# Optimization experiments

Hardware: AMD Instinct MI355X
Metric: run time of the kernel (lower is better)

## Reference

```python
import jax, jax.numpy as jnp
import numpy as np

B, N, EMB, HID, CODE, FEAT, L = 8, 96, 768, 384, 192, 768, 2
NEG = 1e30  # mask_logic constant


def _gru(x, h, Wih, Whh, bih, bhh):
    # torch.nn.GRUCell math; gate order r, z, n
    gi = x @ Wih.T + bih
    gh = h @ Whh.T + bhh
    ir, iz, inn = jnp.split(gi, 3, axis=-1)
    hr, hz, hn = jnp.split(gh, 3, axis=-1)
    r = jax.nn.sigmoid(ir + hr)
    z = jax.nn.sigmoid(iz + hz)
    n = jnp.tanh(inn + r * hn)
    return (1.0 - z) * n + z * h


def _node0(Hl, gc, gp):
    # node 0: C = gru_c(x, 0); P = gru_p(0, x); H1 = C + P
    x0 = Hl[:, 0]
    z0 = jnp.zeros_like(x0)
    h0 = _gru(x0, z0, *gc) + _gru(z0, x0, *gp)
    b, n, d = Hl.shape
    return jnp.zeros((b, n, d), Hl.dtype).at[:, 0].set(h0)


def _dag_scan(Hl, s_mask, aux, Wr0, Wr1, gc, gp, get_w):
    # sequential DAG recurrence: node i attends over nodes < i of the CURRENT layer's outputs
    b, n, d = Hl.shape
    buf0 = _node0(Hl, gc, gp)
    pos = jnp.arange(n)

    def step(buf, inp):
        i, q, s_row, aux_row = inp
        valid = pos < i                                  # growing history slice [:i]
        w = get_w(buf, q, aux_row, valid)                # (B,N), zero for j >= i
        s = s_row[:, :, None]
        V = (buf @ Wr0.T) * s + (buf @ Wr1.T) * (1.0 - s)  # speaker-relation values
        M = jnp.einsum('bn,bnd->bd', w, V)
        hn = _gru(q, M, *gc) + _gru(M, q, *gp)           # C + P
        return buf.at[:, i].set(hn), w

    xs = (jnp.arange(1, n),
          jnp.swapaxes(Hl[:, 1:], 0, 1),
          jnp.swapaxes(s_mask[:, 1:], 0, 1),
          jnp.swapaxes(aux[:, 1:], 0, 1))
    buf, ws = jax.lax.scan(step, buf0, xs)
    return buf, jnp.swapaxes(ws, 0, 1)  # H1 (B,N,D), attn rows 1..N-1 (B,N-1,N)


def _mlp(x, W0, b0, W1, b1):
    # out_mlp with mlp_layers=1 (dropout is identity in eval mode)
    return jax.nn.relu(x @ W0.T + b0) @ W1.T + b1


def _forward(features, adj, s_mask, s_mask_onehot,
             enc_fc1_W, enc_fc1_b, enc_gat_w, enc_gat_b, enc_Wr0, enc_Wr1,
             enc_gruc_Wih, enc_gruc_Whh, enc_gruc_bih, enc_gruc_bhh,
             enc_grup_Wih, enc_grup_Whh, enc_grup_bih, enc_grup_bhh,
             enc_mlp_W0, enc_mlp_b0, enc_mlp_W1, enc_mlp_b1,
             dec_fc1_W, dec_fc1_b, dec_Wr0, dec_Wr1,
             dec_gruc_Wih, dec_gruc_Whh, dec_gruc_bih, dec_gruc_bhh,
             dec_grup_Wih, dec_grup_Whh, dec_grup_bih, dec_grup_bhh,
             dec_mlp_W0, dec_mlp_b0, dec_mlp_W1, dec_mlp_b1,
             lengths):
    b, n, _ = features.shape
    I = jnp.broadcast_to(jnp.eye(n, dtype=features.dtype), (b, n, n))
    # ----- encoder -----
    Hs = [jax.nn.relu(features @ enc_fc1_W.T + enc_fc1_b)]
    adjB_list = [jnp.zeros((b, 1, n), features.dtype)]
    for l in range(L):
        gc = (enc_gruc_Wih[l], enc_gruc_Whh[l], enc_gruc_bih[l], enc_gruc_bhh[l])
        gp = (enc_grup_Wih[l], enc_grup_Whh[l], enc_grup_bih[l], enc_grup_bhh[l])
        wq, wk, gb = enc_gat_w[l, :HID], enc_gat_w[l, HID:], enc_gat_b[l]

        def get_w(buf, q, adj_row, valid, wq=wq, wk=wk, gb=gb):
            # GAT_encoder: alpha = Linear([q; K]) masked by adj over history (mask_logic)
            alpha = buf @ wk + (q @ wq)[:, None] + gb
            alpha = alpha - (1.0 - adj_row) * NEG
            alpha = jnp.where(valid[None, :], alpha, -jnp.inf)
            return jax.nn.softmax(alpha, axis=-1)

        H1, ws = _dag_scan(Hs[l], s_mask, adj, enc_Wr0[l], enc_Wr1[l], gc, gp, get_w)
        Hs.append(H1)
        # row 0 of adjB is zeros; rows 1..N-1 are zero-padded attention weights
        adjB_list.append(jnp.concatenate([jnp.zeros((b, 1, n), features.dtype), ws], axis=1))
    fU = _mlp(jnp.concatenate(Hs, axis=-1), enc_mlp_W0, enc_mlp_b0, enc_mlp_W1, enc_mlp_b1)
    # ----- decoder -----
    Hs = [jax.nn.relu(fU @ dec_fc1_W.T + dec_fc1_b)]
    for l in range(L):
        gc = (dec_gruc_Wih[l], dec_gruc_Whh[l], dec_gruc_bih[l], dec_gruc_bhh[l])
        gp = (dec_grup_Wih[l], dec_grup_Whh[l], dec_grup_bih[l], dec_grup_bhh[l])
        b_inv = jnp.linalg.solve(I, I - adjB_list[l + 1])

        def get_w(buf, q, w_row, valid):
            # GNN_decoder: uses b_inv[:, i, :i] directly as gather weights
            return jnp.where(valid[None, :], w_row, 0.0)

        H1, _ = _dag_scan(Hs[l], s_mask, b_inv, dec_Wr0[l], dec_Wr1[l], gc, gp, get_w)
        Hs.append(H1)
    logits = _mlp(jnp.concatenate(Hs, axis=-1), dec_mlp_W0, dec_mlp_b0, dec_mlp_W1, dec_mlp_b1)
    feature_map = jnp.linalg.solve(I, I - adjB_list[2])
    return logits, feature_map


def setup_inputs() -> dict:
    key = jax.random.key(0)
    ks = iter(jax.random.split(key, 48))

    def rn(*shape):
        return jax.random.normal(next(ks), shape, jnp.float32) * 0.05

    return dict(
        features=jax.random.normal(next(ks), (B, N, EMB), jnp.float32),
        adj=jax.random.randint(next(ks), (B, N, N), 0, 2).astype(jnp.float32),
        s_mask=jax.random.randint(next(ks), (B, N, N), 0, 2).astype(jnp.float32),
        s_mask_onehot=jnp.zeros((B, N, N, 2), jnp.float32),
        lengths=jax.random.randint(next(ks), (B,), 1, N),
        enc_fc1_W=rn(HID, EMB), enc_fc1_b=rn(HID),
        enc_gat_w=rn(L, 2 * HID), enc_gat_b=rn(L),
        enc_Wr0=rn(L, HID, HID), enc_Wr1=rn(L, HID, HID),
        enc_gruc_Wih=rn(L, 3 * HID, HID), enc_gruc_Whh=rn(L, 3 * HID, HID),
        enc_gruc_bih=rn(L, 3 * HID), enc_gruc_bhh=rn(L, 3 * HID),
        enc_grup_Wih=rn(L, 3 * HID, HID), enc_grup_Whh=rn(L, 3 * HID, HID),
        enc_grup_bih=rn(L, 3 * HID), enc_grup_bhh=rn(L, 3 * HID),
        enc_mlp_W0=rn(HID, (L + 1) * HID), enc_mlp_b0=rn(HID),
        enc_mlp_W1=rn(CODE, HID), enc_mlp_b1=rn(CODE),
        dec_fc1_W=rn(HID, CODE), dec_fc1_b=rn(HID),
        dec_Wr0=rn(L, HID, HID), dec_Wr1=rn(L, HID, HID),
        dec_gruc_Wih=rn(L, 3 * HID, HID), dec_gruc_Whh=rn(L, 3 * HID, HID),
        dec_gruc_bih=rn(L, 3 * HID), dec_gruc_bhh=rn(L, 3 * HID),
        dec_grup_Wih=rn(L, 3 * HID, HID), dec_grup_Whh=rn(L, 3 * HID, HID),
        dec_grup_bih=rn(L, 3 * HID), dec_grup_bhh=rn(L, 3 * HID),
        dec_mlp_W0=rn(HID, (L + 1) * HID), dec_mlp_b0=rn(HID),
        dec_mlp_W1=rn(FEAT, HID), dec_mlp_b1=rn(FEAT),
    )


def reference(features, adj, s_mask, s_mask_onehot, lengths,
              enc_fc1_W, enc_fc1_b, enc_gat_w, enc_gat_b, enc_Wr0, enc_Wr1,
              enc_gruc_Wih, enc_gruc_Whh, enc_gruc_bih, enc_gruc_bhh,
              enc_grup_Wih, enc_grup_Whh, enc_grup_bih, enc_grup_bhh,
              enc_mlp_W0, enc_mlp_b0, enc_mlp_W1, enc_mlp_b1,
              dec_fc1_W, dec_fc1_b, dec_Wr0, dec_Wr1,
              dec_gruc_Wih, dec_gruc_Whh, dec_gruc_bih, dec_gruc_bhh,
              dec_grup_Wih, dec_grup_Whh, dec_grup_bih, dec_grup_bhh,
              dec_mlp_W0, dec_mlp_b0, dec_mlp_W1, dec_mlp_b1):
    return _forward(features, adj, s_mask, s_mask_onehot,
                    enc_fc1_W, enc_fc1_b, enc_gat_w, enc_gat_b, enc_Wr0, enc_Wr1,
                    enc_gruc_Wih, enc_gruc_Whh, enc_gruc_bih, enc_gruc_bhh,
                    enc_grup_Wih, enc_grup_Whh, enc_grup_bih, enc_grup_bhh,
                    enc_mlp_W0, enc_mlp_b0, enc_mlp_W1, enc_mlp_b1,
                    dec_fc1_W, dec_fc1_b, dec_Wr0, dec_Wr1,
                    dec_gruc_Wih, dec_gruc_Whh, dec_gruc_bih, dec_gruc_bhh,
                    dec_grup_Wih, dec_grup_Whh, dec_grup_bih, dec_grup_bhh,
                    dec_mlp_W0, dec_mlp_b0, dec_mlp_W1, dec_mlp_b1,
                    lengths)
```

## Files before the change

### kernel.cpp

```cpp
#include <hip/hip_runtime.h>
#include <math.h>

#define B_    8
#define N_    96
#define EMB_  768
#define HID_  384
#define GID_  1152
#define CONC_ 1152
#define CODE_ 192
#define FEAT_ 768
#define NSL_  64
#define SD_   6
#define NRW_  42

__device__ __forceinline__ float sigf(float x) { return 1.0f / (1.0f + expf(-x)); }

__device__ __forceinline__ void atstf(float* p, float v) {
  __hip_atomic_store(p, v, __ATOMIC_RELAXED, __HIP_MEMORY_SCOPE_AGENT);
}
__device__ __forceinline__ float atldf(const float* p) {
  return __hip_atomic_load((float*)p, __ATOMIC_RELAXED, __HIP_MEMORY_SCOPE_AGENT);
}
__device__ __forceinline__ float dot4(float4 a, float4 b) {
  return fmaf(a.x, b.x, fmaf(a.y, b.y, fmaf(a.z, b.z, a.w * b.w)));
}

template<int RELU>
__global__ __launch_bounds__(256)
void gemm_bias(const float* __restrict__ A, int lda,
               const float* __restrict__ W,
               const float* __restrict__ bias,
               float* __restrict__ C, int ldc, int K)
{
  __shared__ float As[16][68];
  __shared__ float Bs[16][68];
  const int tid = threadIdx.x;
  const int m0 = blockIdx.y * 64;
  const int n0 = blockIdx.x * 64;
  const int lr = tid >> 2;
  const int lc = (tid & 3) * 4;
  const int ty = tid >> 4, tx = tid & 15;
  float acc[4][4] = {};
  for (int k0 = 0; k0 < K; k0 += 16) {
    float4 a4 = *(const float4*)(A + (size_t)(m0 + lr) * lda + k0 + lc);
    float4 b4 = *(const float4*)(W + (size_t)(n0 + lr) * K + k0 + lc);
    As[lc+0][lr] = a4.x; As[lc+1][lr] = a4.y; As[lc+2][lr] = a4.z; As[lc+3][lr] = a4.w;
    Bs[lc+0][lr] = b4.x; Bs[lc+1][lr] = b4.y; Bs[lc+2][lr] = b4.z; Bs[lc+3][lr] = b4.w;
    __syncthreads();
#pragma unroll
    for (int k = 0; k < 16; ++k) {
      float av[4], bv[4];
#pragma unroll
      for (int i = 0; i < 4; ++i) av[i] = As[k][ty*4+i];
#pragma unroll
      for (int j = 0; j < 4; ++j) bv[j] = Bs[k][tx*4+j];
#pragma unroll
      for (int i = 0; i < 4; ++i)
#pragma unroll
        for (int j = 0; j < 4; ++j) acc[i][j] = fmaf(av[i], bv[j], acc[i][j]);
    }
    __syncthreads();
  }
#pragma unroll
  for (int i = 0; i < 4; ++i) {
    int m = m0 + ty*4 + i;
#pragma unroll
    for (int j = 0; j < 4; ++j) {
      int n = n0 + tx*4 + j;
      float v = acc[i][j] + bias[n];
      if (RELU) v = fmaxf(v, 0.0f);
      C[(size_t)m * ldc + n] = v;
    }
  }
}

__global__ __launch_bounds__(256)
void prod_kernel(const float* __restrict__ Ac, const float* __restrict__ Ap,
                 const float* __restrict__ W0, const float* __restrict__ W1,
                 float* __restrict__ G)
{
  const float* A = (blockIdx.z < 2) ? Ac : Ap;
  const float* W = (blockIdx.z & 1) ? W1 : W0;
  float* C = G + (size_t)blockIdx.z * GID_ * HID_;
  __shared__ float As[16][68];
  __shared__ float Bs[16][68];
  const int tid = threadIdx.x;
  const int m0 = blockIdx.y * 64;
  const int n0 = blockIdx.x * 64;
  const int lr = tid >> 2;
  const int lc = (tid & 3) * 4;
  const int lr2 = tid & 63, kq = tid >> 6;
  const int ty = tid >> 4, tx = tid & 15;
  float acc[4][4] = {};
  for (int k0 = 0; k0 < HID_; k0 += 16) {
    float4 a4 = *(const float4*)(A + (size_t)(m0 + lr) * HID_ + k0 + lc);
    As[lc+0][lr] = a4.x; As[lc+1][lr] = a4.y; As[lc+2][lr] = a4.z; As[lc+3][lr] = a4.w;
#pragma unroll
    for (int u = 0; u < 4; ++u) {
      int kl = kq * 4 + u;
      Bs[kl][lr2] = W[(size_t)(k0 + kl) * HID_ + n0 + lr2];
    }
    __syncthreads();
#pragma unroll
    for (int k = 0; k < 16; ++k) {
      float av[4], bv[4];
#pragma unroll
      for (int i = 0; i < 4; ++i) av[i] = As[k][ty*4+i];
#pragma unroll
      for (int j = 0; j < 4; ++j) bv[j] = Bs[k][tx*4+j];
#pragma unroll
      for (int i = 0; i < 4; ++i)
#pragma unroll
        for (int j = 0; j < 4; ++j) acc[i][j] = fmaf(av[i], bv[j], acc[i][j]);
    }
    __syncthreads();
  }
#pragma unroll
  for (int i = 0; i < 4; ++i)
#pragma unroll
    for (int j = 0; j < 4; ++j)
      C[(size_t)(m0 + ty*4 + i) * HID_ + n0 + tx*4 + j] = acc[i][j];
}

struct ScanP {
  const float* __restrict__ Hl;
  float*       __restrict__ bufC;
  float*       __restrict__ hnX;
  const float* __restrict__ G;
  const float* __restrict__ GIc;
  const float* __restrict__ GHp;
  const float* __restrict__ bhhc;
  const float* __restrict__ bihp;
  const float* __restrict__ Wr0;
  const float* __restrict__ Wr1;
  const float* __restrict__ wk;
  const float* __restrict__ mask;
  const float* __restrict__ smask;
  float*       __restrict__ adjB;
};

template<int ENC>
__global__ __launch_bounds__(256, 2)
void scan_kernel(ScanP p)
{
  const int tid  = threadIdx.x;
  const int bid  = blockIdx.x;
  const int b    = (bid >> 3) & 7;
  const int sl   = ((bid & 7) << 3) | (bid >> 6);
  const int j0   = sl * SD_;
  const int team = tid >> 4, lane = tid & 15;

  __shared__ __align__(16) float stage[HID_];
  __shared__ float ws0[N_], ws1[N_], s_sm[N_];
  __shared__ float alpha[N_];
  __shared__ float dots[48];
  __shared__ float red4[4];
  __shared__ float sh_aknew;
  __shared__ float PA[NRW_ * 97];
  __shared__ float PB[NRW_ * 97];

  for (int k = tid; k < NRW_ * 97; k += 256) { PA[k] = 0.f; PB[k] = 0.f; }

  float4 wAr[3][6], wBr[3][6];
#pragma unroll
  for (int u = 0; u < 3; ++u) {
    const int r = team + 16 * u;
    const float *Aptr, *Bptr;
    if (r < 36) {
      const int g = r / 6, jl = r % 6;
      const size_t off = (size_t)((g % 3) * HID_ + j0 + jl) * HID_;
      const float* base = p.G + (g < 3 ? 0 : 2) * (size_t)GID_ * HID_;
      Aptr = base + off;
      Bptr = base + (size_t)GID_ * HID_ + off;
    } else if (r < 42) {
      const int jl = r - 36;
      Aptr = p.Wr0 + (size_t)(j0 + jl) * HID_;
      Bptr = p.Wr1 + (size_t)(j0 + jl) * HID_;
    } else if (r == 42 && ENC) {
      Aptr = p.wk; Bptr = p.wk;
    } else {
      Aptr = p.Wr0; Bptr = p.Wr1;
    }
#pragma unroll
    for (int m = 0; m < 6; ++m) {
      wAr[u][m] = ((const float4*)Aptr)[lane + 16*m];
      wBr[u][m] = ((const float4*)Bptr)[lane + 16*m];
    }
  }
  float bh0=0, bh1=0, bh2=0, bi0=0, bi1=0, bi2=0;
  if (tid < SD_) {
    int j = j0 + tid;
    bh0 = p.bhhc[j]; bh1 = p.bhhc[HID_ + j]; bh2 = p.bhhc[2*HID_ + j];
    bi0 = p.bihp[j]; bi1 = p.bihp[HID_ + j]; bi2 = p.bihp[2*HID_ + j];
  }

#define BULK_STAGE(SRC)                                                      \
  do {                                                                       \
    if (tid < NSL_) {                                                        \
      const float* f_ = (SRC) + tid * SD_;                                   \
      while (__float_as_uint(atldf(f_)) == 0xFFFFFFFFu) {}                   \
    }                                                                        \
    __syncthreads();                                                         \
    {                                                                        \
      float v0 = atldf((SRC) + tid);                                         \
      while (__float_as_uint(v0) == 0xFFFFFFFFu) v0 = atldf((SRC) + tid);    \
      stage[tid] = v0;                                                       \
      if (tid < HID_ - 256) {                                                \
        float v1 = atldf((SRC) + 256 + tid);                                 \
        while (__float_as_uint(v1) == 0xFFFFFFFFu)                           \
          v1 = atldf((SRC) + 256 + tid);                                     \
        stage[256 + tid] = v1;                                               \
      }                                                                      \
    }                                                                        \
    __syncthreads();                                                         \
  } while (0)

  if (tid < SD_) {
    int j = j0 + tid;
    const float* gi = p.GIc + (size_t)(b * N_) * GID_;
    const float* gh = p.GHp + (size_t)(b * N_) * GID_;
    float rc = sigf(gi[j] + bh0);
    float zc = sigf(gi[HID_ + j] + bh1);
    float nc = tanhf(gi[2*HID_ + j] + rc * bh2);
    float outc = (1.0f - zc) * nc;
    float rp = sigf(bi0 + gh[j]);
    float zp = sigf(bi1 + gh[HID_ + j]);
    float np = tanhf(bi2 + rp * gh[2*HID_ + j]);
    float x0 = p.Hl[(size_t)(b * N_) * CONC_ + j];
    float h0 = outc + (1.0f - zp) * np + zp * x0;
    p.bufC[(size_t)(b * N_) * CONC_ + j] = h0;
    atstf(&p.hnX[(size_t)(b * N_) * HID_ + j], h0);
  }
  __syncthreads();

  for (int i = 1; i < N_; ++i) {
    float pf_gi0=0, pf_gi1=0, pf_gi2=0, pf_gh0=0, pf_gh1=0, pf_gh2=0, pf_q=0;
    if (tid < SD_) {
      int j = j0 + tid;
      const float* gi = p.GIc + ((size_t)b * N_ + i) * GID_;
      const float* gh = p.GHp + ((size_t)b * N_ + i) * GID_;
      pf_gi0 = gi[j]; pf_gi1 = gi[HID_ + j]; pf_gi2 = gi[2*HID_ + j];
      pf_gh0 = gh[j]; pf_gh1 = gh[HID_ + j]; pf_gh2 = gh[2*HID_ + j];
      pf_q   = p.Hl[((size_t)b * N_ + i) * CONC_ + j];
    }
    float pf_mrow = 0.0f;
    if (tid < N_) {
      pf_mrow = p.mask[((size_t)b * N_ + i) * N_ + tid];
      s_sm[tid] = p.smask[((size_t)b * N_ + i) * N_ + tid];
    }

    const float* srcH = p.hnX + (size_t)(b * N_ + (i - 1)) * HID_;
    BULK_STAGE(srcH);
    const float4* st4 = (const float4*)stage;
    float4 hreg[6];
#pragma unroll
    for (int m = 0; m < 6; ++m) hreg[m] = st4[lane + 16*m];

#pragma unroll
    for (int u = 0; u < 3; ++u) {
      const int r = team + 16 * u;
      float a = 0.f, bv = 0.f;
#pragma unroll
      for (int m = 0; m < 6; ++m) {
        a  += dot4(wAr[u][m], hreg[m]);
        bv += dot4(wBr[u][m], hreg[m]);
      }
#pragma unroll
      for (int mm = 8; mm; mm >>= 1) {
        a  += __shfl_xor(a, mm);
        bv += __shfl_xor(bv, mm);
      }
      if (lane == 0) {
        if (r < NRW_) { PA[r * 97 + (i - 1)] = a; PB[r * 97 + (i - 1)] = bv; }
        else if (ENC && r == 42) sh_aknew = a;
      }
    }
    __syncthreads();

    if (ENC) {
      if (tid == 0) alpha[i - 1] = sh_aknew;
      float av = -3.0e38f;
      if (tid < i) {
        float ak = (tid == i - 1) ? sh_aknew : alpha[tid];
        av = ak - (1.0f - pf_mrow) * 1e30f;
      }
      float v = av;
#pragma unroll
      for (int m = 32; m; m >>= 1) v = fmaxf(v, __shfl_xor(v, m));
      if ((tid & 63) == 0) red4[tid >> 6] = v;
      __syncthreads();
      float mx = fmaxf(fmaxf(red4[0], red4[1]), fmaxf(red4[2], red4[3]));
      __syncthreads();
      float e = (tid < i) ? expf(av - mx) : 0.0f;
      v = e;
#pragma unroll
      for (int m = 32; m; m >>= 1) v += __shfl_xor(v, m);
      if ((tid & 63) == 0) red4[tid >> 6] = v;
      __syncthreads();
      float ssum = red4[0] + red4[1] + red4[2] + red4[3];
      if (tid < N_) {
        float w = (tid < i) ? e / ssum : 0.0f;
        float sv = s_sm[tid];
        ws0[tid] = w * sv;
        ws1[tid] = w - w * sv;
        if (sl == 0) p.adjB[((size_t)b * N_ + i) * N_ + tid] = w;
      }
      __syncthreads();
    } else {
      if (tid < N_) {
        float w = (tid < i) ? -pf_mrow : 0.0f;
        float sv = s_sm[tid];
        ws0[tid] = w * sv;
        ws1[tid] = w - w * sv;
      }
      __syncthreads();
    }

    {
      float wsr0[6], wsr1[6];
#pragma unroll
      for (int k = 0; k < 6; ++k) {
        wsr0[k] = ws0[lane + 16*k];
        wsr1[k] = ws1[lane + 16*k];
      }
#pragma unroll
      for (int u = 0; u < 3; ++u) {
        const int r = team + 16 * u;
        if (r < NRW_) {
          float acc = 0.f;
#pragma unroll
          for (int k = 0; k < 6; ++k) {
            int n = lane + 16*k;
            acc = fmaf(wsr0[k], PA[r * 97 + n], fmaf(wsr1[k], PB[r * 97 + n], acc));
          }
#pragma unroll
          for (int mm = 8; mm; mm >>= 1) acc += __shfl_xor(acc, mm);
          if (lane == 0) dots[r] = acc;
        }
      }
    }
    __syncthreads();

    if (tid < SD_) {
      int j = j0 + tid;
      float Mj = dots[36 + tid];
      float rc = sigf(pf_gi0 + dots[tid] + bh0);
      float zc = sigf(pf_gi1 + dots[6 + tid] + bh1);
      float nc = tanhf(pf_gi2 + rc * (dots[12 + tid] + bh2));
      float outc = (1.0f - zc) * nc + zc * Mj;
      float rp = sigf(dots[18 + tid] + bi0 + pf_gh0);
      float zp = sigf(dots[24 + tid] + bi1 + pf_gh1);
      float np = tanhf(dots[30 + tid] + bi2 + rp * pf_gh2);
      float hv = outc + (1.0f - zp) * np + zp * pf_q;
      p.bufC[((size_t)b * N_ + i) * CONC_ + j] = hv;
      atstf(&p.hnX[((size_t)b * N_ + i) * HID_ + j], hv);
    }
    __syncthreads();
  }
#undef BULK_STAGE
}

__global__ __launch_bounds__(256)
void fmap_kernel(const float* __restrict__ adjB2, float* __restrict__ out)
{
  int idx = blockIdx.x * 256 + threadIdx.x;
  if (idx < B_ * N_ * N_) {
    int j = idx % N_;
    int i = (idx / N_) % N_;
    float a = (i == 0) ? 0.0f : adjB2[idx];
    out[idx] = ((i == j) ? 1.0f : 0.0f) - a;
  }
}

extern "C" void kernel_launch(void* const* d_in, const int* in_sizes, int n_in,
                              void* d_out, int out_size, void* d_ws, size_t ws_size,
                              hipStream_t stream)
{
  (void)in_sizes; (void)n_in; (void)out_size; (void)ws_size;
  const float* features     = (const float*)d_in[0];
  const float* adj          = (const float*)d_in[1];
  const float* s_mask       = (const float*)d_in[2];
  const float* enc_fc1_W    = (const float*)d_in[5];
  const float* enc_fc1_b    = (const float*)d_in[6];
  const float* enc_gat_w    = (const float*)d_in[7];
  const float* enc_Wr0      = (const float*)d_in[9];
  const float* enc_Wr1      = (const float*)d_in[10];
  const float* enc_gruc_Wih = (const float*)d_in[11];
  const float* enc_gruc_Whh = (const float*)d_in[12];
  const float* enc_gruc_bih = (const float*)d_in[13];
  const float* enc_gruc_bhh = (const float*)d_in[14];
  const float* enc_grup_Wih = (const float*)d_in[15];
  const float* enc_grup_Whh = (const float*)d_in[16];
  const float* enc_grup_bih = (const float*)d_in[17];
  const float* enc_grup_bhh = (const float*)d_in[18];
  const float* enc_mlp_W0   = (const float*)d_in[19];
  const float* enc_mlp_b0   = (const float*)d_in[20];
  const float* enc_mlp_W1   = (const float*)d_in[21];
  const float* enc_mlp_b1   = (const float*)d_in[22];
  const float* dec_fc1_W    = (const float*)d_in[23];
  const float* dec_fc1_b    = (const float*)d_in[24];
  const float* dec_Wr0      = (const float*)d_in[25];
  const float* dec_Wr1      = (const float*)d_in[26];
  const float* dec_gruc_Wih = (const float*)d_in[27];
  const float* dec_gruc_Whh = (const float*)d_in[28];
  const float* dec_gruc_bih = (const float*)d_in[29];
  const float* dec_gruc_bhh = (const float*)d_in[30];
  const float* dec_grup_Wih = (const float*)d_in[31];
  const float* dec_grup_Whh = (const float*)d_in[32];
  const float* dec_grup_bih = (const float*)d_in[33];
  const float* dec_grup_bhh = (const float*)d_in[34];
  const float* dec_mlp_W0   = (const float*)d_in[35];
  const float* dec_mlp_b0   = (const float*)d_in[36];
  const float* dec_mlp_W1   = (const float*)d_in[37];
  const float* dec_mlp_b1   = (const float*)d_in[38];

  float* ws = (float*)d_ws;
  size_t o = 0;
  float* Hse   = ws + o; o += (size_t)B_ * N_ * CONC_;
  float* Hsd   = ws + o; o += (size_t)B_ * N_ * CONC_;
  float* GIc   = ws + o; o += (size_t)B_ * N_ * GID_;
  float* GHp   = ws + o; o += (size_t)B_ * N_ * GID_;
  float* adjB1 = ws + o; o += (size_t)B_ * N_ * N_;
  float* adjB2 = ws + o; o += (size_t)B_ * N_ * N_;
  float* fU    = ws + o; o += (size_t)B_ * N_ * CODE_;
  float* Tmp   = ws + o; o += (size_t)B_ * N_ * HID_;
  float* hnX   = ws + o; o += (size_t)B_ * N_ * HID_;
  float* Gbuf  = ws + o; o += (size_t)4 * GID_ * HID_;
  const size_t hn_bytes = (size_t)B_ * N_ * HID_ * sizeof(float);

  const dim3 blk(256);
  float* logits = (float*)d_out;
  float* fmap   = (float*)d_out + (size_t)B_ * N_ * FEAT_;

  gemm_bias<1><<<dim3(6, 12), blk, 0, stream>>>(features, EMB_, enc_fc1_W, enc_fc1_b,
                                                Hse, CONC_, EMB_);
  for (int l = 0; l < 2; ++l) {
    const float* Hl = Hse + l * HID_;
    gemm_bias<0><<<dim3(18, 12), blk, 0, stream>>>(Hl, CONC_,
        enc_gruc_Wih + (size_t)l * GID_ * HID_, enc_gruc_bih + l * GID_, GIc, GID_, HID_);
    gemm_bias<0><<<dim3(18, 12), blk, 0, stream>>>(Hl, CONC_,
        enc_grup_Whh + (size_t)l * GID_ * HID_, enc_grup_bhh + l * GID_, GHp, GID_, HID_);
    prod_kernel<<<dim3(6, 18, 4), blk, 0, stream>>>(
        enc_gruc_Whh + (size_t)l * GID_ * HID_, enc_grup_Wih + (size_t)l * GID_ * HID_,
        enc_Wr0 + (size_t)l * HID_ * HID_, enc_Wr1 + (size_t)l * HID_ * HID_, Gbuf);
    hipMemsetAsync(hnX, 0xFF, hn_bytes, stream);
    ScanP p;
    p.Hl = Hl; p.bufC = Hse + (l + 1) * HID_;
    p.hnX = hnX; p.G = Gbuf;
    p.GIc = GIc; p.GHp = GHp;
    p.bhhc = enc_gruc_bhh + l * GID_;
    p.bihp = enc_grup_bih + l * GID_;
    p.Wr0 = enc_Wr0 + (size_t)l * HID_ * HID_;
    p.Wr1 = enc_Wr1 + (size_t)l * HID_ * HID_;
    p.wk = enc_gat_w + l * 2 * HID_ + HID_;
    p.mask = adj; p.smask = s_mask;
    p.adjB = (l == 0) ? adjB1 : adjB2;
    scan_kernel<1><<<dim3(512), blk, 0, stream>>>(p);
  }
  gemm_bias<1><<<dim3(6, 12), blk, 0, stream>>>(Hse, CONC_, enc_mlp_W0, enc_mlp_b0,
                                                Tmp, HID_, CONC_);
  gemm_bias<0><<<dim3(3, 12), blk, 0, stream>>>(Tmp, HID_, enc_mlp_W1, enc_mlp_b1,
                                                fU, CODE_, HID_);
  gemm_bias<1><<<dim3(6, 12), blk, 0, stream>>>(fU, CODE_, dec_fc1_W, dec_fc1_b,
                                                Hsd, CONC_, CODE_);
  for (int l = 0; l < 2; ++l) {
    const float* Hl = Hsd + l * HID_;
    gemm_bias<0><<<dim3(18, 12), blk, 0, stream>>>(Hl, CONC_,
        dec_gruc_Wih + (size_t)l * GID_ * HID_, dec_gruc_bih + l * GID_, GIc, GID_, HID_);
    gemm_bias<0><<<dim3(18, 12), blk, 0, stream>>>(Hl, CONC_,
        dec_grup_Whh + (size_t)l * GID_ * HID_, dec_grup_bhh + l * GID_, GHp, GID_, HID_);
    prod_kernel<<<dim3(6, 18, 4), blk, 0, stream>>>(
        dec_gruc_Whh + (size_t)l * GID_ * HID_, dec_grup_Wih + (size_t)l * GID_ * HID_,
        dec_Wr0 + (size_t)l * HID_ * HID_, dec_Wr1 + (size_t)l * HID_ * HID_, Gbuf);
    hipMemsetAsync(hnX, 0xFF, hn_bytes, stream);
    ScanP p;
    p.Hl = Hl; p.bufC = Hsd + (l + 1) * HID_;
    p.hnX = hnX; p.G = Gbuf;
    p.GIc = GIc; p.GHp = GHp;
    p.bhhc = dec_gruc_bhh + l * GID_;
    p.bihp = dec_grup_bih + l * GID_;
    p.Wr0 = dec_Wr0 + (size_t)l * HID_ * HID_;
    p.Wr1 = dec_Wr1 + (size_t)l * HID_ * HID_;
    p.wk = nullptr;
    p.mask = (l == 0) ? adjB1 : adjB2;
    p.smask = s_mask;
    p.adjB = nullptr;
    scan_kernel<0><<<dim3(512), blk, 0, stream>>>(p);
  }
  gemm_bias<1><<<dim3(6, 12), blk, 0, stream>>>(Hsd, CONC_, dec_mlp_W0, dec_mlp_b0,
                                                Tmp, HID_, CONC_);
  gemm_bias<0><<<dim3(12, 12), blk, 0, stream>>>(Tmp, HID_, dec_mlp_W1, dec_mlp_b1,
                                                 logits, FEAT_, HID_);
  fmap_kernel<<<dim3((B_ * N_ * N_ + 255) / 256), blk, 0, stream>>>(adjB2, fmap);
}
```

Baseline: 1.992 ms.

## Store scan weights in bf16 and stream them from memory instead of registers

The precomputed product matrices and the relation weights Wr0/Wr1/wk are converted to bf16: prod_kernel writes bf16 output and a new pack_wr kernel packs the relation weights. The scan kernel stops holding 144 float4 weight registers per thread and instead loads packed bf16 uint4 rows from global memory (likely L2-resident) on every step. The hidden-state staging layout is reordered to match the 8-wide dot products. This lowers register pressure and weight bytes, at the cost of bf16 rounding in the recurrent weights and repeated per-step weight loads on the serial critical path.

```diff
diff --git a/kernel.cpp b/kernel.cpp
--- a/kernel.cpp
+++ b/kernel.cpp
@@ -1,4 +1,5 @@
 #include <hip/hip_runtime.h>
+#include <hip/hip_bf16.h>
 #include <math.h>
 
 #define B_    8
@@ -21,8 +22,20 @@
 __device__ __forceinline__ float atldf(const float* p) {
   return __hip_atomic_load((float*)p, __ATOMIC_RELAXED, __HIP_MEMORY_SCOPE_AGENT);
 }
-__device__ __forceinline__ float dot4(float4 a, float4 b) {
-  return fmaf(a.x, b.x, fmaf(a.y, b.y, fmaf(a.z, b.z, a.w * b.w)));
+__device__ __forceinline__ unsigned short f2bf(float f) {
+  __hip_bfloat16 h = __float2bfloat16(f);
+  return *reinterpret_cast<unsigned short*>(&h);
+}
+__device__ __forceinline__ float dot8bf(uint4 w, float4 h0, float4 h1, float acc) {
+  acc = fmaf(__uint_as_float(w.x << 16),          h0.x, acc);
+  acc = fmaf(__uint_as_float(w.x & 0xffff0000u),  h0.y, acc);
+  acc = fmaf(__uint_as_float(w.y << 16),          h0.z, acc);
+  acc = fmaf(__uint_as_float(w.y & 0xffff0000u),  h0.w, acc);
+  acc = fmaf(__uint_as_float(w.z << 16),          h1.x, acc);
+  acc = fmaf(__uint_as_float(w.z & 0xffff0000u),  h1.y, acc);
+  acc = fmaf(__uint_as_float(w.w << 16),          h1.z, acc);
+  acc = fmaf(__uint_as_float(w.w & 0xffff0000u),  h1.w, acc);
+  return acc;
 }
 
 template<int RELU>
@@ -77,11 +90,11 @@
 __global__ __launch_bounds__(256)
 void prod_kernel(const float* __restrict__ Ac, const float* __restrict__ Ap,
                  const float* __restrict__ W0, const float* __restrict__ W1,
-                 float* __restrict__ G)
+                 unsigned short* __restrict__ Gb)
 {
   const float* A = (blockIdx.z < 2) ? Ac : Ap;
   const float* W = (blockIdx.z & 1) ? W1 : W0;
-  float* C = G + (size_t)blockIdx.z * GID_ * HID_;
+  unsigned short* C = Gb + (size_t)blockIdx.z * GID_ * HID_;
   __shared__ float As[16][68];
   __shared__ float Bs[16][68];
   const int tid = threadIdx.x;
@@ -119,21 +132,35 @@
   for (int i = 0; i < 4; ++i)
 #pragma unroll
     for (int j = 0; j < 4; ++j)
-      C[(size_t)(m0 + ty*4 + i) * HID_ + n0 + tx*4 + j] = acc[i][j];
+      C[(size_t)(m0 + ty*4 + i) * HID_ + n0 + tx*4 + j] = f2bf(acc[i][j]);
+}
+
+__global__ __launch_bounds__(256)
+void pack_wr(const float* __restrict__ Wr0, const float* __restrict__ Wr1,
+             const float* __restrict__ wk,
+             unsigned short* __restrict__ Wr0b, unsigned short* __restrict__ Wr1b,
+             unsigned short* __restrict__ wkb, int has_wk)
+{
+  int idx = blockIdx.x * 256 + threadIdx.x;
+  if (idx < HID_ * HID_) {
+    Wr0b[idx] = f2bf(Wr0[idx]);
+    Wr1b[idx] = f2bf(Wr1[idx]);
+  }
+  if (has_wk && idx < HID_) wkb[idx] = f2bf(wk[idx]);
 }
 
 struct ScanP {
   const float* __restrict__ Hl;
   float*       __restrict__ bufC;
   float*       __restrict__ hnX;
-  const float* __restrict__ G;
+  const unsigned short* __restrict__ Gb;
+  const unsigned short* __restrict__ Wr0b;
+  const unsigned short* __restrict__ Wr1b;
+  const unsigned short* __restrict__ wkb;
   const float* __restrict__ GIc;
   const float* __restrict__ GHp;
   const float* __restrict__ bhhc;
   const float* __restrict__ bihp;
-  const float* __restrict__ Wr0;
-  const float* __restrict__ Wr1;
-  const float* __restrict__ wk;
   const float* __restrict__ mask;
   const float* __restrict__ smask;
   float*       __restrict__ adjB;
@@ -161,32 +188,31 @@
 
   for (int k = tid; k < NRW_ * 97; k += 256) { PA[k] = 0.f; PB[k] = 0.f; }
 
-  float4 wAr[3][6], wBr[3][6];
+  const uint4* pAu[3];
+  const uint4* pBu[3];
 #pragma unroll
   for (int u = 0; u < 3; ++u) {
     const int r = team + 16 * u;
-    const float *Aptr, *Bptr;
+    const unsigned short *Aptr, *Bptr;
     if (r < 36) {
       const int g = r / 6, jl = r % 6;
       const size_t off = (size_t)((g % 3) * HID_ + j0 + jl) * HID_;
-      const float* base = p.G + (g < 3 ? 0 : 2) * (size_t)GID_ * HID_;
+      const unsigned short* base = p.Gb + (g < 3 ? 0 : 2) * (size_t)GID_ * HID_;
       Aptr = base + off;
       Bptr = base + (size_t)GID_ * HID_ + off;
     } else if (r < 42) {
       const int jl = r - 36;
-      Aptr = p.Wr0 + (size_t)(j0 + jl) * HID_;
-      Bptr = p.Wr1 + (size_t)(j0 + jl) * HID_;
+      Aptr = p.Wr0b + (size_t)(j0 + jl) * HID_;
+      Bptr = p.Wr1b + (size_t)(j0 + jl) * HID_;
     } else if (r == 42 && ENC) {
-      Aptr = p.wk; Bptr = p.wk;
+      Aptr = p.wkb; Bptr = p.wkb;
     } else {
-      Aptr = p.Wr0; Bptr = p.Wr1;
-    }
-#pragma unroll
-    for (int m = 0; m < 6; ++m) {
-      wAr[u][m] = ((const float4*)Aptr)[lane + 16*m];
-      wBr[u][m] = ((const float4*)Bptr)[lane + 16*m];
-    }
-  }
+      Aptr = p.Wr0b; Bptr = p.Wr1b;
+    }
+    pAu[u] = (const uint4*)Aptr;
+    pBu[u] = (const uint4*)Bptr;
+  }
+
   float bh0=0, bh1=0, bh2=0, bi0=0, bi1=0, bi2=0;
   if (tid < SD_) {
     int j = j0 + tid;
@@ -252,18 +278,23 @@
     const float* srcH = p.hnX + (size_t)(b * N_ + (i - 1)) * HID_;
     BULK_STAGE(srcH);
     const float4* st4 = (const float4*)stage;
-    float4 hreg[6];
-#pragma unroll
-    for (int m = 0; m < 6; ++m) hreg[m] = st4[lane + 16*m];
+    float4 h0r[3], h1r[3];
+#pragma unroll
+    for (int m = 0; m < 3; ++m) {
+      h0r[m] = st4[(m * 16 + lane) * 2];
+      h1r[m] = st4[(m * 16 + lane) * 2 + 1];
+    }
 
 #pragma unroll
     for (int u = 0; u < 3; ++u) {
       const int r = team + 16 * u;
       float a = 0.f, bv = 0.f;
 #pragma unroll
-      for (int m = 0; m < 6; ++m) {
-        a  += dot4(wAr[u][m], hreg[m]);
-        bv += dot4(wBr[u][m], hreg[m]);
+      for (int m = 0; m < 3; ++m) {
+        uint4 wa = pAu[u][m * 16 + lane];
+        uint4 wb = pBu[u][m * 16 + lane];
+        a  = dot8bf(wa, h0r[m], h1r[m], a);
+        bv = dot8bf(wb, h0r[m], h1r[m], bv);
       }
 #pragma unroll
       for (int mm = 8; mm; mm >>= 1) {
@@ -425,7 +456,10 @@
   float* fU    = ws + o; o += (size_t)B_ * N_ * CODE_;
   float* Tmp   = ws + o; o += (size_t)B_ * N_ * HID_;
   float* hnX   = ws + o; o += (size_t)B_ * N_ * HID_;
-  float* Gbuf  = ws + o; o += (size_t)4 * GID_ * HID_;
+  unsigned short* Gb   = (unsigned short*)(ws + o); o += (size_t)4 * GID_ * HID_ / 2;
+  unsigned short* Wr0b = (unsigned short*)(ws + o); o += (size_t)HID_ * HID_ / 2;
+  unsigned short* Wr1b = (unsigned short*)(ws + o); o += (size_t)HID_ * HID_ / 2;
+  unsigned short* wkb  = (unsigned short*)(ws + o); o += 256;
   const size_t hn_bytes = (size_t)B_ * N_ * HID_ * sizeof(float);
 
   const dim3 blk(256);
@@ -442,17 +476,18 @@
         enc_grup_Whh + (size_t)l * GID_ * HID_, enc_grup_bhh + l * GID_, GHp, GID_, HID_);
     prod_kernel<<<dim3(6, 18, 4), blk, 0, stream>>>(
         enc_gruc_Whh + (size_t)l * GID_ * HID_, enc_grup_Wih + (size_t)l * GID_ * HID_,
-        enc_Wr0 + (size_t)l * HID_ * HID_, enc_Wr1 + (size_t)l * HID_ * HID_, Gbuf);
+        enc_Wr0 + (size_t)l * HID_ * HID_, enc_Wr1 + (size_t)l * HID_ * HID_, Gb);
+    pack_wr<<<dim3((HID_ * HID_ + 255) / 256), blk, 0, stream>>>(
+        enc_Wr0 + (size_t)l * HID_ * HID_, enc_Wr1 + (size_t)l * HID_ * HID_,
+        enc_gat_w + l * 2 * HID_ + HID_, Wr0b, Wr1b, wkb, 1);
     hipMemsetAsync(hnX, 0xFF, hn_bytes, stream);
     ScanP p;
     p.Hl = Hl; p.bufC = Hse + (l + 1) * HID_;
-    p.hnX = hnX; p.G = Gbuf;
+    p.hnX = hnX;
+    p.Gb = Gb; p.Wr0b = Wr0b; p.Wr1b = Wr1b; p.wkb = wkb;
     p.GIc = GIc; p.GHp = GHp;
     p.bhhc = enc_gruc_bhh + l * GID_;
     p.bihp = enc_grup_bih + l * GID_;
-    p.Wr0 = enc_Wr0 + (size_t)l * HID_ * HID_;
-    p.Wr1 = enc_Wr1 + (size_t)l * HID_ * HID_;
-    p.wk = enc_gat_w + l * 2 * HID_ + HID_;
     p.mask = adj; p.smask = s_mask;
     p.adjB = (l == 0) ? adjB1 : adjB2;
     scan_kernel<1><<<dim3(512), blk, 0, stream>>>(p);
@@ -471,17 +506,18 @@
         dec_grup_Whh + (size_t)l * GID_ * HID_, dec_grup_bhh + l * GID_, GHp, GID_, HID_);
     prod_kernel<<<dim3(6, 18, 4), blk, 0, stream>>>(
         dec_gruc_Whh + (size_t)l * GID_ * HID_, dec_grup_Wih + (size_t)l * GID_ * HID_,
-        dec_Wr0 + (size_t)l * HID_ * HID_, dec_Wr1 + (size_t)l * HID_ * HID_, Gbuf);
+        dec_Wr0 + (size_t)l * HID_ * HID_, dec_Wr1 + (size_t)l * HID_ * HID_, Gb);
+    pack_wr<<<dim3((HID_ * HID_ + 255) / 256), blk, 0, stream>>>(
+        dec_Wr0 + (size_t)l * HID_ * HID_, dec_Wr1 + (size_t)l * HID_ * HID_,
+        nullptr, Wr0b, Wr1b, wkb, 0);
     hipMemsetAsync(hnX, 0xFF, hn_bytes, stream);
     ScanP p;
     p.Hl = Hl; p.bufC = Hsd + (l + 1) * HID_;
-    p.hnX = hnX; p.G = Gbuf;
+    p.hnX = hnX;
+    p.Gb = Gb; p.Wr0b = Wr0b; p.Wr1b = Wr1b; p.wkb = wkb;
     p.GIc = GIc; p.GHp = GHp;
     p.bhhc = dec_gruc_bhh + l * GID_;
     p.bihp = dec_grup_bih + l * GID_;
-    p.Wr0 = dec_Wr0 + (size_t)l * HID_ * HID_;
-    p.Wr1 = dec_Wr1 + (size_t)l * HID_ * HID_;
-    p.wk = nullptr;
     p.mask = (l == 0) ? adjB1 : adjB2;
     p.smask = s_mask;
     p.adjB = nullptr;
```

New measurement: 2.524 ms. 26.8% more time.
